# Kernel tuning notes

Measured on AMD Instinct MI355X. Metric: run time of the kernel, lower is better.

Reference implementation:

```python
import jax, jax.numpy as jnp
import numpy as np

N_NODES = 100000
N_EDGES = 1600000
N_CLUSTERS = 1024
EPS = 1e-5


def gcn_conv(x, W, b, src, dst, n, ew=None):
    """PyG GCNConv: symmetric norm with self-loops. ew: optional edge weight/mask."""
    h = x @ W
    if ew is None:
        ew = jnp.ones(src.shape[0], h.dtype)
    deg = jax.ops.segment_sum(ew, dst, num_segments=n) + 1.0  # +1 self loop
    dinv = jax.lax.rsqrt(deg)
    coef = dinv[src] * dinv[dst] * ew  # [E]
    out = jax.ops.segment_sum(h[src] * coef[:, None], dst, num_segments=n)
    out = out + h * (dinv * dinv)[:, None]  # self-loop messages
    return out + b


def instance_norm(x):
    # PyG InstanceNorm, batch=None -> single graph, no affine, biased variance
    mu = jnp.mean(x, axis=0, keepdims=True)
    var = jnp.mean((x - mu) ** 2, axis=0, keepdims=True)
    return (x - mu) * jax.lax.rsqrt(var + EPS)


def forward(x, WG1, bG1, WfG1, bfG1, WG2, bG2, WfG2, bfG2,
            WL1, bL1, WfL1, bfL1, WL2, bL2, WfL2, bfL2,
            WO1, bO1, WfO1, bfO1, WO2, bO2, WfO2, bfO2, WO3, bO3, WfO3, bfO3,
            adj, in_batch, cluster):
    elu = jax.nn.elu
    n = x.shape[0]
    src, dst = adj[0], adj[1]
    # global GCN stack
    h = elu(gcn_conv(x, WG1, bG1, src, dst, n))
    h = elu(h @ WfG1 + bfG1)
    h = elu(gcn_conv(h, WG2, bG2, src, dst, n))
    h = elu(h @ WfG2 + bfG2)
    y = instance_norm(h)  # [N, 256]
    # avg_pool over clusters (single graph -> batch offset is 0 but kept faithful)
    bc = cluster + in_batch * N_CLUSTERS  # [N]
    cnt = jax.ops.segment_sum(jnp.ones(n, y.dtype), bc, num_segments=N_CLUSTERS)
    px = jax.ops.segment_sum(y, bc, num_segments=N_CLUSTERS) / jnp.maximum(cnt, 1.0)[:, None]
    # pool edges: map through cluster, remove self-loops, coalesce (dedupe via sort+mask)
    psrc, pdst = bc[src], bc[dst]
    key = psrc * N_CLUSTERS + pdst
    order = jnp.argsort(key)
    ks = key[order]
    s2, d2 = psrc[order], pdst[order]
    first = jnp.concatenate([jnp.ones((1,), bool), ks[1:] != ks[:-1]])
    emask = (first & (s2 != d2)).astype(y.dtype)
    # local GCN stack on compressed graph
    lx = elu(gcn_conv(px, WL1, bL1, s2, d2, N_CLUSTERS, emask))
    lx = elu(lx @ WfL1 + bfL1)
    lx = elu(gcn_conv(lx, WL2, bL2, s2, d2, N_CLUSTERS, emask))
    lx = elu(lx @ WfL2 + bfL2)  # [C, 64]
    # gather-broadcast compressed features back to nodes
    comp = lx[bc]  # [N, 64]
    z = jnp.concatenate([y, comp], axis=1)  # [N, 320]
    z = elu(gcn_conv(z, WO1, bO1, src, dst, n))
    z = elu(z @ WfO1 + bfO1)
    z = elu(gcn_conv(z, WO2, bO2, src, dst, n))
    z = elu(z @ WfO2 + bfO2)
    z = elu(gcn_conv(z, WO3, bO3, src, dst, n))
    z = elu(z @ WfO3 + bfO3)
    return z


def _lin(key, i, o):
    k1, k2 = jax.random.split(key)
    s = 1.0 / np.sqrt(i)
    return (jax.random.normal(k1, (i, o), jnp.float32) * s,
            jax.random.normal(k2, (o,), jnp.float32) * s)


def setup_inputs() -> dict:
    key = jax.random.key(0)
    ks = jax.random.split(key, 20)
    inp = {}
    inp['x'] = jax.random.normal(ks[0], (N_NODES, 3), jnp.float32)
    inp['adj'] = jax.random.randint(ks[1], (2, N_EDGES), 0, N_NODES, jnp.int64 if jax.config.jax_enable_x64 else jnp.int32)
    inp['num_graphs'] = 1
    inp['in_batch'] = jnp.zeros((N_NODES,), jnp.int32)
    inp['cluster'] = jax.random.randint(ks[2], (N_NODES,), 0, N_CLUSTERS, jnp.int32)
    dims = [('G1', 3, 64), ('fG1', 64, 64), ('G2', 64, 256), ('fG2', 256, 256),
            ('L1', 256, 128), ('fL1', 128, 128), ('L2', 128, 64), ('fL2', 64, 64),
            ('O1', 320, 128), ('fO1', 128, 128), ('O2', 128, 32), ('fO2', 32, 32),
            ('O3', 32, 3), ('fO3', 3, 3)]
    for j, (name, i, o) in enumerate(dims):
        W, b = _lin(ks[3 + j], i, o)
        inp['W' + name] = W
        inp['b' + name] = b
    return inp


def reference(x, adj, num_graphs, in_batch, cluster,
              WG1, bG1, WfG1, bfG1, WG2, bG2, WfG2, bfG2,
              WL1, bL1, WfL1, bfL1, WL2, bL2, WfL2, bfL2,
              WO1, bO1, WfO1, bfO1, WO2, bO2, WfO2, bfO2, WO3, bO3, WfO3, bfO3):
    return forward(x, WG1, bG1, WfG1, bfG1, WG2, bG2, WfG2, bfG2,
                   WL1, bL1, WfL1, bfL1, WL2, bL2, WfL2, bfL2,
                   WO1, bO1, WfO1, bfO1, WO2, bO2, WfO2, bfO2,
                   WO3, bO3, WfO3, bfO3, adj, in_batch, cluster)
```

## Files before the change

kernel.cpp:

```cpp
#include <hip/hip_runtime.h>


#define NCLUST 1024

typedef short bf16x8 __attribute__((ext_vector_type(8)));
typedef float f32x4 __attribute__((ext_vector_type(4)));

__device__ __forceinline__ float elu1(float x) { return x > 0.f ? x : expm1f(x); }

__device__ __forceinline__ unsigned f2bf(float f) {
    union { float f; unsigned u; } c; c.f = f;
    unsigned u = c.u;
    return (u + 0x7fffu + ((u >> 16) & 1u)) >> 16;
}
__device__ __forceinline__ float bf2f(unsigned h) {
    union { unsigned u; float f; } c; c.u = h << 16; return c.f;
}

union U8 { unsigned u[4]; bf16x8 v; };

__device__ __forceinline__ void wpack_body(const float* W, unsigned* Phi, unsigned* Plo,
                                           int K, int BN, int t) {
    int NT = BN / 16;
    int lane = t & 63;
    int rest = t >> 6;
    int ct = rest % NT;
    int s = rest / NT;
    int col = ct * 16 + (lane & 15);
    int g = lane >> 4;
    int k0 = s * 32;
    float e[8];
#pragma unroll
    for (int j = 0; j < 4; j++) {
        e[j]     = W[(size_t)(k0 + 4 * g + j) * BN + col];
        e[4 + j] = W[(size_t)(k0 + 16 + 4 * g + j) * BN + col];
    }
#pragma unroll
    for (int j = 0; j < 4; j++) {
        unsigned h0 = f2bf(e[2 * j]), h1 = f2bf(e[2 * j + 1]);
        Phi[(size_t)t * 4 + j] = h0 | (h1 << 16);
        unsigned l0 = f2bf(e[2 * j] - bf2f(h0));
        unsigned l1 = f2bf(e[2 * j + 1] - bf2f(h1));
        Plo[(size_t)t * 4 + j] = l0 | (l1 << 16);
    }
}

struct PackDesc { const float* W; unsigned* Ph; unsigned* Pl; int K, BN, tbase; };
struct InitArgs {
    PackDesc d[6]; int tot;
    int4* z1; int nz1; int4* z2; int nz2;
};

__global__ void k_init(InitArgs a) {
    int t = blockIdx.x * 256 + threadIdx.x;
    if (t < a.nz1) a.z1[t] = make_int4(0, 0, 0, 0);
    else if (t - a.nz1 < a.nz2) a.z2[t - a.nz1] = make_int4(0, 0, 0, 0);
    if (t < a.tot) {
        int i = 0;
#pragma unroll
        for (int j = 1; j < 6; j++) if (t >= a.d[j].tbase) i = j;
        wpack_body(a.d[i].W, a.d[i].Ph, a.d[i].Pl, a.d[i].K, a.d[i].BN,
                   t - a.d[i].tbase);
    }
}

__global__ void k_hist(const int* __restrict__ key, int* __restrict__ deg, int E) {
    int e = blockIdx.x * 256 + threadIdx.x;
    if (e < E) atomicAdd(&deg[key[e]], 1);
}

__global__ void k_scan_block(const int* __restrict__ deg, int* __restrict__ rowptr,
                             int* __restrict__ bsum, int n) {
    __shared__ int lds[256];
    int tid = threadIdx.x;
    int base = blockIdx.x * 1024 + tid * 4;
    int v0 = base + 0 < n ? deg[base + 0] : 0;
    int v1 = base + 1 < n ? deg[base + 1] : 0;
    int v2 = base + 2 < n ? deg[base + 2] : 0;
    int v3 = base + 3 < n ? deg[base + 3] : 0;
    int tsum = v0 + v1 + v2 + v3;
    lds[tid] = tsum; __syncthreads();
    for (int off = 1; off < 256; off <<= 1) {
        int t = (tid >= off) ? lds[tid - off] : 0;
        __syncthreads();
        lds[tid] += t;
        __syncthreads();
    }
    int run = lds[tid] - tsum;
    if (base + 0 < n) rowptr[base + 0] = run; run += v0;
    if (base + 1 < n) rowptr[base + 1] = run; run += v1;
    if (base + 2 < n) rowptr[base + 2] = run; run += v2;
    if (base + 3 < n) rowptr[base + 3] = run;
    if (tid == 255) bsum[blockIdx.x] = lds[255];
}

__global__ void k_nodeinit(int* __restrict__ rowptr, const int* __restrict__ bsum,
                           const int* __restrict__ deg, const int* __restrict__ cluster,
                           const int* __restrict__ inb, float* __restrict__ dinv,
                           int* __restrict__ bc, int* __restrict__ cdeg, int n, int nb) {
    __shared__ int pfx[128];
    int tid = threadIdx.x;
    if (tid < 128) pfx[tid] = (tid < nb) ? bsum[tid] : 0;
    __syncthreads();
    for (int off = 1; off < 128; off <<= 1) {
        int v = 0;
        if (tid < 128 && tid >= off) v = pfx[tid - off];
        __syncthreads();
        if (tid < 128) pfx[tid] += v;
        __syncthreads();
    }
    int i = blockIdx.x * 256 + tid;
    if (i >= n) return;
    int j = i >> 10;
    int base = (j == 0) ? 0 : pfx[j - 1];
    rowptr[i] += base;
    dinv[i] = rsqrtf((float)deg[i] + 1.0f);
    int c = cluster[i] + inb[i] * NCLUST;
    bc[i] = c;
    atomicAdd(&cdeg[c], 1);
}

__global__ void k_fillc(const int* __restrict__ src, const int* __restrict__ dst,
                        const float* __restrict__ dinv, const int* __restrict__ rowptr,
                        int* __restrict__ fill, int2* __restrict__ csr_ev, int E,
                        const int* __restrict__ bc, const int* __restrict__ crowptr,
                        int* __restrict__ cfill, int* __restrict__ cnodes, int n) {
    int e = blockIdx.x * 256 + threadIdx.x;
    if (e < E) {
        int d = dst[e];
        int pos = rowptr[d] + atomicAdd(&fill[d], 1);
        int s = src[e];
        csr_ev[pos] = make_int2(s, __float_as_int(dinv[s]));
    }
    if (e < n) {
        int c = bc[e];
        int pos = crowptr[c] + atomicAdd(&cfill[c], 1);
        cnodes[pos] = e;
    }
}

template <int F, int OB>
__global__ __launch_bounds__(256) void k_prop4sb(
        const unsigned short* __restrict__ hbf, const float* __restrict__ dinv,
        const int* __restrict__ rowptr, const int* __restrict__ deg,
        const int2* __restrict__ csr_ev,
        const float* __restrict__ bias, float* __restrict__ outf,
        unsigned short* __restrict__ outb, int n, int flags) {
    constexpr int FS = F / 4;
    constexpr int ES = 64 / FS;
    const int node = (blockIdx.x * 256 + threadIdx.x) >> 6;
    if (node >= n) return;
    const int l = threadIdx.x & 63;
    const int fs = l & (FS - 1);
    const int ep = l / FS;
    const int fi = fs * 4;
    const int start = rowptr[node];
    const int cnt = deg[node];
    float ax = 0.f, ay = 0.f, az = 0.f, aw = 0.f;
    for (int j = ep; j < cnt; j += ES) {
        const int2 ev = csr_ev[start + j];
        int s = ev.x;
        float w = __int_as_float(ev.y);
        const ushort4 v = *reinterpret_cast<const ushort4*>(&hbf[(size_t)s * F + fi]);
        ax += w * bf2f(v.x); ay += w * bf2f(v.y);
        az += w * bf2f(v.z); aw += w * bf2f(v.w);
    }
#pragma unroll
    for (int off = FS; off < 64; off <<= 1) {
        ax += __shfl_xor(ax, off);
        ay += __shfl_xor(ay, off);
        az += __shfl_xor(az, off);
        aw += __shfl_xor(aw, off);
    }
    if (ep == 0) {
        float di = dinv[node];
        const ushort4 sv = *reinterpret_cast<const ushort4*>(&hbf[(size_t)node * F + fi]);
        float4 o;
        o.x = di * ax + di * di * bf2f(sv.x);
        o.y = di * ay + di * di * bf2f(sv.y);
        o.z = di * az + di * di * bf2f(sv.z);
        o.w = di * aw + di * di * bf2f(sv.w);
        if (flags) {
            const float4 b = *reinterpret_cast<const float4*>(&bias[fi]);
            o.x = elu1(o.x + b.x); o.y = elu1(o.y + b.y);
            o.z = elu1(o.z + b.z); o.w = elu1(o.w + b.w);
        }
        if constexpr (OB) {
            ushort4 ob;
            ob.x = (unsigned short)f2bf(o.x); ob.y = (unsigned short)f2bf(o.y);
            ob.z = (unsigned short)f2bf(o.z); ob.w = (unsigned short)f2bf(o.w);
            *reinterpret_cast<ushort4*>(&outb[(size_t)node * F + fi]) = ob;
        } else {
            *reinterpret_cast<float4*>(&outf[(size_t)node * F + fi]) = o;
        }
    }
}

__global__ void k_prop3f1(const float* __restrict__ h, const float* __restrict__ dinv,
                          const int* __restrict__ rowptr, const int* __restrict__ deg,
                          const int2* __restrict__ csr_ev,
                          const float* __restrict__ WG1, const float* __restrict__ bG1,
                          unsigned short* __restrict__ outb, int n) {
    int node = blockIdx.x * 256 + threadIdx.x;
    if (node >= n) return;
    int start = rowptr[node], cnt = deg[node];
    float a0 = 0.f, a1 = 0.f, a2 = 0.f;
    for (int j = 0; j < cnt; j++) {
        const int2 ev = csr_ev[start + j];
        int s = ev.x;
        float w = __int_as_float(ev.y);
        a0 += w * h[(size_t)s * 3 + 0];
        a1 += w * h[(size_t)s * 3 + 1];
        a2 += w * h[(size_t)s * 3 + 2];
    }
    float di = dinv[node];
    float p0 = di * a0 + di * di * h[(size_t)node * 3 + 0];
    float p1 = di * a1 + di * di * h[(size_t)node * 3 + 1];
    float p2 = di * a2 + di * di * h[(size_t)node * 3 + 2];
    unsigned short* op = outb + (size_t)node * 64;
#pragma unroll 4
    for (int c = 0; c < 64; c += 4) {
        ushort4 ob;
        ob.x = (unsigned short)f2bf(elu1(p0 * WG1[c + 0] + p1 * WG1[64 + c + 0] + p2 * WG1[128 + c + 0] + bG1[c + 0]));
        ob.y = (unsigned short)f2bf(elu1(p0 * WG1[c + 1] + p1 * WG1[64 + c + 1] + p2 * WG1[128 + c + 1] + bG1[c + 1]));
        ob.z = (unsigned short)f2bf(elu1(p0 * WG1[c + 2] + p1 * WG1[64 + c + 2] + p2 * WG1[128 + c + 2] + bG1[c + 2]));
        ob.w = (unsigned short)f2bf(elu1(p0 * WG1[c + 3] + p1 * WG1[64 + c + 3] + p2 * WG1[128 + c + 3] + bG1[c + 3]));
        *reinterpret_cast<ushort4*>(op + c) = ob;
    }
}

__global__ void k_prop3out(const float* __restrict__ h, const float* __restrict__ dinv,
                           const int* __restrict__ rowptr, const int* __restrict__ deg,
                           const int2* __restrict__ csr_ev,
                           const float* __restrict__ bO3, const float* __restrict__ WfO3,
                           const float* __restrict__ bfO3, float* __restrict__ out, int n) {
    int node = blockIdx.x * 256 + threadIdx.x;
    if (node >= n) return;
    int start = rowptr[node], cnt = deg[node];
    float a0 = 0.f, a1 = 0.f, a2 = 0.f;
    for (int j = 0; j < cnt; j++) {
        const int2 ev = csr_ev[start + j];
        int s = ev.x;
        float w = __int_as_float(ev.y);
        a0 += w * h[(size_t)s * 3 + 0];
        a1 += w * h[(size_t)s * 3 + 1];
        a2 += w * h[(size_t)s * 3 + 2];
    }
    float di = dinv[node];
    float o0 = elu1(di * a0 + di * di * h[(size_t)node * 3 + 0] + bO3[0]);
    float o1 = elu1(di * a1 + di * di * h[(size_t)node * 3 + 1] + bO3[1]);
    float o2 = elu1(di * a2 + di * di * h[(size_t)node * 3 + 2] + bO3[2]);
#pragma unroll
    for (int c = 0; c < 3; c++) {
        out[(size_t)node * 3 + c] =
            elu1(o0 * WfO3[c] + o1 * WfO3[3 + c] + o2 * WfO3[6 + c] + bfO3[c]);
    }
}

__global__ void k_normprep(const float* __restrict__ W, const float* __restrict__ insum,
                           const float* __restrict__ insumsq, unsigned* __restrict__ Phi,
                           unsigned* __restrict__ Plo, float* __restrict__ corr,
                           float* __restrict__ mu, float* __restrict__ rstd, int n) {
    const float fn = (float)n;
    const int bid = blockIdx.x, tid = threadIdx.x;
    if (bid == 16) {
        float m = insum[tid] / fn;
        float var = insumsq[tid] / fn - m * m;
        mu[tid] = m;
        rstd[tid] = rsqrtf(var + 1e-5f);
        return;
    }
    {
        int t = bid * 256 + tid;
        int lane = t & 63, rest = t >> 6;
        int ct = rest % 8, s = rest / 8;
        int col = ct * 16 + (lane & 15);
        int g = lane >> 4;
        int k0 = s * 32;
        float e[8];
#pragma unroll
        for (int j = 0; j < 4; j++) {
            int ka = k0 + 4 * g + j;
            int kb = k0 + 16 + 4 * g + j;
            float ma = insum[ka] / fn;
            float sa = rsqrtf(insumsq[ka] / fn - ma * ma + 1e-5f);
            float mb = insum[kb] / fn;
            float sb = rsqrtf(insumsq[kb] / fn - mb * mb + 1e-5f);
            e[j]     = W[(size_t)ka * 128 + col] * sa;
            e[4 + j] = W[(size_t)kb * 128 + col] * sb;
        }
#pragma unroll
        for (int j = 0; j < 4; j++) {
            unsigned h0 = f2bf(e[2 * j]), h1 = f2bf(e[2 * j + 1]);
            Phi[(size_t)t * 4 + j] = h0 | (h1 << 16);
            unsigned l0 = f2bf(e[2 * j] - bf2f(h0));
            unsigned l1 = f2bf(e[2 * j + 1] - bf2f(h1));
            Plo[(size_t)t * 4 + j] = l0 | (l1 << 16);
        }
    }
    if (tid < 128) {
        int k0 = bid * 16;
        float s = 0.f;
        for (int k = k0; k < k0 + 16; k++) {
            float m = insum[k] / fn;
            float r = rsqrtf(insumsq[k] / fn - m * m + 1e-5f);
            s += m * r * W[(size_t)k * 128 + tid];
        }
        atomicAdd(&corr[tid], s);
    }
}

template <int BN, int WAVES>
__global__ __launch_bounds__(WAVES * 64) void k_gmfma(
        const unsigned short* __restrict__ Abf,
        const unsigned* __restrict__ Phi, const unsigned* __restrict__ Plo,
        const float* __restrict__ bias, const float* __restrict__ sub,
        const float* __restrict__ add, const int* __restrict__ addidx,
        float* __restrict__ C, unsigned short* __restrict__ Cbf,
        int N, int K, int flags) {
    constexpr int NT = BN / 16;
    constexpr int WCOL = (BN == 256) ? 4 : (BN == 128 ? 2 : 1);
    constexpr int WROW = WAVES / WCOL;
    constexpr int NTW = NT / WCOL;
    constexpr int BR = 32 * WROW;
    constexpr bool LDSW = (BN >= 128);
    __shared__ unsigned lds_w[LDSW ? 2 * 2 * NT * 256 : 1];
    const int t = threadIdx.x;
    const int w = t >> 6, l = t & 63;
    const int wr = w / WCOL, wc = w % WCOL;
    const int l15 = l & 15, g = l >> 4;
    const int row0 = blockIdx.x * BR + wr * 32;
    const int ctbase = wc * NTW;
    int ar0 = row0 + l15;      ar0 = ar0 < N ? ar0 : N - 1;
    int ar1 = row0 + 16 + l15; ar1 = ar1 < N ? ar1 : N - 1;
    const unsigned short* ab0 = Abf + (size_t)ar0 * K;
    const unsigned short* ab1 = Abf + (size_t)ar1 * K;

    f32x4 acc[2][NTW];
#pragma unroll
    for (int f = 0; f < 2; f++)
#pragma unroll
        for (int ct = 0; ct < NTW; ct++) acc[f][ct] = (f32x4){0.f, 0.f, 0.f, 0.f};

    auto loadA = [&](int s, U8* ahi) {
        const int k0 = s * 32;
#pragma unroll
        for (int f = 0; f < 2; f++) {
            const unsigned short* ab = f ? ab1 : ab0;
            const uint2 hA = *reinterpret_cast<const uint2*>(ab + k0 + 4 * g);
            const uint2 hB = *reinterpret_cast<const uint2*>(ab + k0 + 16 + 4 * g);
            ahi[f].u[0] = hA.x; ahi[f].u[1] = hA.y;
            ahi[f].u[2] = hB.x; ahi[f].u[3] = hB.y;
        }
    };
    auto domfma = [&](U8* wh, U8* wl, U8* ahi) {
#pragma unroll
        for (int ct = 0; ct < NTW; ct++) {
            acc[0][ct] = __builtin_amdgcn_mfma_f32_16x16x32_bf16(ahi[0].v, wh[ct].v, acc[0][ct], 0, 0, 0);
            acc[0][ct] = __builtin_amdgcn_mfma_f32_16x16x32_bf16(ahi[0].v, wl[ct].v, acc[0][ct], 0, 0, 0);
            acc[1][ct] = __builtin_amdgcn_mfma_f32_16x16x32_bf16(ahi[1].v, wh[ct].v, acc[1][ct], 0, 0, 0);
            acc[1][ct] = __builtin_amdgcn_mfma_f32_16x16x32_bf16(ahi[1].v, wl[ct].v, acc[1][ct], 0, 0, 0);
        }
    };

    const int nk = K / 32;

    if constexpr (LDSW) {
        auto stage = [&](int s, int b) {
            unsigned* base = lds_w + (size_t)b * (2 * NT * 256);
            for (int i = w; i < 2 * NT; i += WAVES) {
                const unsigned* gsrc = (i < NT)
                    ? Phi + (size_t)(s * NT + i) * 256 + l * 4
                    : Plo + (size_t)(s * NT + (i - NT)) * 256 + l * 4;
                __builtin_amdgcn_global_load_lds(
                    (const __attribute__((address_space(1))) unsigned*)gsrc,
                    (__attribute__((address_space(3))) unsigned*)(base + i * 256),
                    16, 0, 0);
            }
        };
        auto loadWlds = [&](int b, U8* wh, U8* wl) {
            const unsigned* base = lds_w + (size_t)b * (2 * NT * 256);
#pragma unroll
            for (int ct = 0; ct < NTW; ct++) {
                wh[ct] = *reinterpret_cast<const U8*>(base + (ctbase + ct) * 256 + l * 4);
                wl[ct] = *reinterpret_cast<const U8*>(base + (NT + ctbase + ct) * 256 + l * 4);
            }
        };

        U8 wh[NTW], wl[NTW], ahiA[2], ahiB[2];
        stage(0, 0);
        loadA(0, ahiA);
        __syncthreads();
        int s = 0;
        while (true) {
            const bool hasB = (s + 1 < nk);
            if (hasB) { stage(s + 1, (s + 1) & 1); loadA(s + 1, ahiB); }
            loadWlds(s & 1, wh, wl);
            domfma(wh, wl, ahiA);
            __syncthreads();
            if (!hasB) break;
            s++;
            const bool hasA2 = (s + 1 < nk);
            if (hasA2) { stage(s + 1, (s + 1) & 1); loadA(s + 1, ahiA); }
            loadWlds(s & 1, wh, wl);
            domfma(wh, wl, ahiB);
            __syncthreads();
            if (!hasA2) break;
            s++;
        }
    } else {
        auto loadW = [&](int s, U8* wh, U8* wl) {
            const unsigned* pb = Phi + ((size_t)(s * NT + ctbase) * 64 + l) * 4;
            const unsigned* pl = Plo + ((size_t)(s * NT + ctbase) * 64 + l) * 4;
#pragma unroll
            for (int ct = 0; ct < NTW; ct++) {
                wh[ct] = *reinterpret_cast<const U8*>(pb + (size_t)ct * 256);
                wl[ct] = *reinterpret_cast<const U8*>(pl + (size_t)ct * 256);
            }
        };
        U8 whA[NTW], wlA[NTW], ahiA[2];
        U8 whB[NTW], wlB[NTW], ahiB[2];
        loadW(0, whA, wlA);
        loadA(0, ahiA);
        int s = 0;
        while (true) {
            const bool hasB = (s + 1 < nk);
            if (hasB) { loadW(s + 1, whB, wlB); loadA(s + 1, ahiB); }
            domfma(whA, wlA, ahiA);
            if (!hasB) break;
            const bool hasA2 = (s + 2 < nk);
            if (hasA2) { loadW(s + 2, whA, wlA); loadA(s + 2, ahiA); }
            domfma(whB, wlB, ahiB);
            if (!hasA2) break;
            s += 2;
        }
        __syncthreads();
    }

#pragma unroll
    for (int f = 0; f < 2; f++) {
#pragma unroll
        for (int r = 0; r < 4; r++) {
            int row = row0 + 16 * f + 4 * g + r;
            if (row >= N) continue;
            int gi = (add != nullptr) ? addidx[row] : 0;
#pragma unroll
            for (int ct = 0; ct < NTW; ct++) {
                int col = (ctbase + ct) * 16 + l15;
                float o = acc[f][ct][r];
                if (add != nullptr) o += add[(size_t)gi * BN + col];
                if (sub != nullptr) o -= sub[col];
                if (flags) o = elu1(o + bias[col]);
                if (C != nullptr) C[(size_t)row * BN + col] = o;
                if (Cbf != nullptr) Cbf[(size_t)row * BN + col] = (unsigned short)f2bf(o);
            }
        }
    }
}

template <int M, int RPT>
__global__ __launch_bounds__(256) void k_fc(
        const float* __restrict__ A, const float* __restrict__ W,
        const float* __restrict__ bias, const float* __restrict__ add,
        const int* __restrict__ addidx, float* __restrict__ C,
        int N, int K, int flags) {
    constexpr int TX = M / 4;
    constexpr int TY = 256 / TX;
    constexpr int RB = TY * RPT;
    int tx = threadIdx.x % TX;
    int ty = threadIdx.x / TX;
    int row0 = blockIdx.x * RB + ty * RPT;
    float4 acc[RPT];
#pragma unroll
    for (int r = 0; r < RPT; r++) acc[r] = make_float4(0.f, 0.f, 0.f, 0.f);
    for (int k = 0; k < K; k++) {
        float4 w = *reinterpret_cast<const float4*>(&W[(size_t)k * M + tx * 4]);
#pragma unroll
        for (int r = 0; r < RPT; r++) {
            int row = row0 + r;
            row = row < N ? row : N - 1;
            float a = A[(size_t)row * K + k];
            acc[r].x += a * w.x; acc[r].y += a * w.y;
            acc[r].z += a * w.z; acc[r].w += a * w.w;
        }
    }
    if (add != nullptr) {
#pragma unroll
        for (int r = 0; r < RPT; r++) {
            int row = row0 + r;
            if (row < N) {
                int g = addidx[row];
                const float4 v = *reinterpret_cast<const float4*>(&add[(size_t)g * M + tx * 4]);
                acc[r].x += v.x; acc[r].y += v.y; acc[r].z += v.z; acc[r].w += v.w;
            }
        }
    }
    __syncthreads();
    float4 b = make_float4(0.f, 0.f, 0.f, 0.f);
    if (flags) b = *reinterpret_cast<const float4*>(&bias[tx * 4]);
#pragma unroll
    for (int r = 0; r < RPT; r++) {
        int row = row0 + r;
        if (row >= N) break;
        float4 o = acc[r];
        o.x += b.x; o.y += b.y; o.z += b.z; o.w += b.w;
        if (flags) { o.x = elu1(o.x); o.y = elu1(o.y); o.z = elu1(o.z); o.w = elu1(o.w); }
        *reinterpret_cast<float4*>(&C[(size_t)row * M + tx * 4]) = o;
    }
}

__global__ __launch_bounds__(256) void k_fcl2(
        const float* __restrict__ A, const float* __restrict__ W1,
        const float* __restrict__ b1, const float* __restrict__ W2,
        float* __restrict__ lxout, float* __restrict__ compO) {
    __shared__ float lx[32][64];
    const int tid = threadIdx.x;
    const int tx = tid % 16, ty = tid / 16;
    const int row0b = blockIdx.x * 32;
    float4 acc[2];
    acc[0] = make_float4(0.f, 0.f, 0.f, 0.f);
    acc[1] = make_float4(0.f, 0.f, 0.f, 0.f);
    for (int k = 0; k < 64; k++) {
        float4 w = *reinterpret_cast<const float4*>(&W1[(size_t)k * 64 + tx * 4]);
#pragma unroll
        for (int r = 0; r < 2; r++) {
            float a = A[(size_t)(row0b + ty * 2 + r) * 64 + k];
            acc[r].x += a * w.x; acc[r].y += a * w.y;
            acc[r].z += a * w.z; acc[r].w += a * w.w;
        }
    }
    float4 b = *reinterpret_cast<const float4*>(&b1[tx * 4]);
#pragma unroll
    for (int r = 0; r < 2; r++) {
        int lr = ty * 2 + r;
        float4 o;
        o.x = elu1(acc[r].x + b.x); o.y = elu1(acc[r].y + b.y);
        o.z = elu1(acc[r].z + b.z); o.w = elu1(acc[r].w + b.w);
        *reinterpret_cast<float4*>(&lxout[(size_t)(row0b + lr) * 64 + tx * 4]) = o;
        lx[lr][tx * 4 + 0] = o.x; lx[lr][tx * 4 + 1] = o.y;
        lx[lr][tx * 4 + 2] = o.z; lx[lr][tx * 4 + 3] = o.w;
    }
    __syncthreads();
    for (int o = tid; o < 32 * 128; o += 256) {
        int r = o >> 7, c = o & 127;
        float s = 0.f;
        for (int k = 0; k < 64; k++) s += lx[r][k] * W2[(size_t)k * 128 + c];
        compO[(size_t)(row0b + r) * 128 + c] = s;
    }
}

__global__ void k_fc3(const float* __restrict__ A, const float* __restrict__ W,
                      const float* __restrict__ b, float* __restrict__ C,
                      int n, int K, int flags) {
    int r = blockIdx.x * 256 + threadIdx.x;
    if (r >= n) return;
    float a0 = 0.f, a1 = 0.f, a2 = 0.f;
    for (int k = 0; k < K; k++) {
        float a = A[(size_t)r * K + k];
        a0 += a * W[k * 3 + 0]; a1 += a * W[k * 3 + 1]; a2 += a * W[k * 3 + 2];
    }
    if (flags) {
        a0 = elu1(a0 + b[0]); a1 = elu1(a1 + b[1]); a2 = elu1(a2 + b[2]);
    }
    C[(size_t)r * 3 + 0] = a0;
    C[(size_t)r * 3 + 1] = a1;
    C[(size_t)r * 3 + 2] = a2;
}

__global__ void k_instats(const unsigned short* __restrict__ h, float* __restrict__ sum,
                          float* __restrict__ sumsq, int n) {
    int c = threadIdx.x;
    int r0 = blockIdx.x * 128;
    int r1 = r0 + 128 < n ? r0 + 128 : n;
    float s = 0.f, q = 0.f;
    for (int r = r0; r < r1; r++) {
        float v = bf2f(h[(size_t)r * 256 + c]);
        s += v; q += v * v;
    }
    atomicAdd(&sum[c], s);
    atomicAdd(&sumsq[c], q);
}

__global__ __launch_bounds__(256) void k_poolmerge(
        const unsigned short* __restrict__ xh, const int* __restrict__ crowptr,
        const int* __restrict__ cdeg, const int* __restrict__ cnodes,
        const float* __restrict__ mu, const float* __restrict__ rstd,
        float* __restrict__ px,
        const int* __restrict__ src, const int* __restrict__ dst,
        const int* __restrict__ bc, unsigned char* __restrict__ bmT, int E) {
    int bid = blockIdx.x;
    if (bid < NCLUST) {
        int cl = bid;
        int c  = threadIdx.x;
        int start = crowptr[cl];
        int cnt = cdeg[cl];
        float acc = 0.f;
        for (int j = 0; j < cnt; j++) {
            int node = cnodes[start + j];
            acc += bf2f(xh[(size_t)node * 256 + c]);
        }
        float res = acc / fmaxf((float)cnt, 1.0f);
        res = (cnt > 0) ? (res - mu[c]) * rstd[c] : 0.f;
        px[(size_t)cl * 256 + c] = res;
    } else {
        int e = (bid - NCLUST) * 256 + threadIdx.x;
        if (e < E) {
            int ps = bc[src[e]];
            int pd = bc[dst[e]];
            bmT[(size_t)pd * NCLUST + ps] = 1;
        }
    }
}

__global__ __launch_bounds__(256) void k_pooldeg(
        const unsigned char* __restrict__ bmT, float* __restrict__ dinvp) {
    int d = blockIdx.x;
    int t = threadIdx.x;
    const unsigned int v = reinterpret_cast<const unsigned int*>(bmT + (size_t)d * NCLUST)[t];
    int s = (v & 0xff) + ((v >> 8) & 0xff) + ((v >> 16) & 0xff) + ((v >> 24) & 0xff);
    if (t == (d >> 2)) s -= (v >> ((d & 3) * 8)) & 0xff;
    __shared__ int red[256];
    red[t] = s; __syncthreads();
    for (int o = 128; o > 0; o >>= 1) {
        if (t < o) red[t] += red[t + o];
        __syncthreads();
    }
    if (t == 0) dinvp[d] = rsqrtf((float)red[0] + 1.0f);
}

template <int F>
__global__ __launch_bounds__(1024) void k_proppool2(
        const float* __restrict__ h, const float* __restrict__ dinvp,
        const unsigned char* __restrict__ bmT, const float* __restrict__ bias,
        float* __restrict__ out) {
    constexpr int SG = 1024 / F;
    const int d = blockIdx.x;
    const int t = threadIdx.x;
    const int f = t & (F - 1);
    const int sg = t / F;
    const unsigned char* bmrow = bmT + (size_t)d * NCLUST;
    float acc = 0.f;
#pragma unroll 4
    for (int s = sg; s < NCLUST; s += SG) {
        float m = (s != d) ? (float)bmrow[s] : 0.f;
        acc += m * dinvp[s] * h[(size_t)s * F + f];
    }
    __shared__ float red[1024];
    red[t] = acc; __syncthreads();
#pragma unroll
    for (int o = SG / 2; o > 0; o >>= 1) {
        if (sg < o) red[t] += red[t + o * F];
        __syncthreads();
    }
    if (sg == 0) {
        float di = dinvp[d];
        float r = di * red[f] + di * di * h[(size_t)d * F + f] + bias[f];
        out[(size_t)d * F + f] = elu1(r);
    }
}

extern "C" void kernel_launch(void* const* d_in, const int* in_sizes, int n_in,
                              void* d_out, int out_size, void* d_ws, size_t ws_size,
                              hipStream_t stream) {
    const float* x       = (const float*)d_in[0];
    const int*   adj     = (const int*)d_in[1];
    const int*   inb     = (const int*)d_in[3];
    const int*   cluster = (const int*)d_in[4];
    const float* WG1  = (const float*)d_in[5];   const float* bG1  = (const float*)d_in[6];
    const float* WfG1 = (const float*)d_in[7];   const float* bfG1 = (const float*)d_in[8];
    const float* WG2  = (const float*)d_in[9];   const float* bG2  = (const float*)d_in[10];
    const float* WfG2 = (const float*)d_in[11];  const float* bfG2 = (const float*)d_in[12];
    const float* WL1  = (const float*)d_in[13];  const float* bL1  = (const float*)d_in[14];
    const float* WfL1 = (const float*)d_in[15];  const float* bfL1 = (const float*)d_in[16];
    const float* WL2  = (const float*)d_in[17];  const float* bL2  = (const float*)d_in[18];
    const float* WfL2 = (const float*)d_in[19];  const float* bfL2 = (const float*)d_in[20];
    const float* WO1  = (const float*)d_in[21];  const float* bO1  = (const float*)d_in[22];
    const float* WfO1 = (const float*)d_in[23];  const float* bfO1 = (const float*)d_in[24];
    const float* WO2  = (const float*)d_in[25];  const float* bO2  = (const float*)d_in[26];
    const float* WfO2 = (const float*)d_in[27];  const float* bfO2 = (const float*)d_in[28];
    const float* WO3  = (const float*)d_in[29];  const float* bO3  = (const float*)d_in[30];
    const float* WfO3 = (const float*)d_in[31];  const float* bfO3 = (const float*)d_in[32];
    float* out = (float*)d_out;

    const int n = in_sizes[0] / 3;
    const int E = in_sizes[1] / 2;
    const int* src = adj;
    const int* dst = adj + E;

    char* ws = (char*)d_ws;
    size_t off = 0;
    auto alloc = [&](size_t bytes) -> void* {
        void* p = ws + off;
        off = (off + bytes + 255) & ~(size_t)255;
        return p;
    };
    int*   deg     = (int*)alloc((size_t)n * 4);
    int*   fill    = (int*)alloc((size_t)n * 4);
    int*   cdeg    = (int*)alloc(NCLUST * 4);
    int*   cfill   = (int*)alloc(NCLUST * 4);
    int*   rowptr  = (int*)alloc((size_t)n * 4);
    int*   crowptr = (int*)alloc(NCLUST * 4);
    int*   cnodes  = (int*)alloc((size_t)n * 4);
    int*   bcarr   = (int*)alloc((size_t)n * 4);
    float* dinv    = (float*)alloc((size_t)n * 4);
    int*   bsum    = (int*)alloc(512);
    int2*  csr_ev  = (int2*)alloc((size_t)E * 8);
    float* X       = (float*)alloc((size_t)n * 256 * 4);
    unsigned short* Xh = (unsigned short*)alloc((size_t)n * 256 * 2);
    float* B       = (float*)alloc((size_t)n * 128 * 4);
    unsigned short* Bh = (unsigned short*)alloc((size_t)n * 128 * 2);
    float* insum   = (float*)alloc(256 * 4);
    float* insumsq = (float*)alloc(256 * 4);
    float* px      = (float*)alloc((size_t)NCLUST * 256 * 4);
    unsigned char* bmT = (unsigned char*)alloc((size_t)NCLUST * NCLUST);
    float* corr    = (float*)alloc(128 * 4);
    float* mu      = (float*)alloc(256 * 4);
    float* rstd    = (float*)alloc(256 * 4);
    float* dinvp   = (float*)alloc(NCLUST * 4);
    float* lA      = (float*)alloc((size_t)NCLUST * 128 * 4);
    float* lB      = (float*)alloc((size_t)NCLUST * 128 * 4);
    unsigned* pfG1h = (unsigned*)alloc(2048 * 4);   unsigned* pfG1l = (unsigned*)alloc(2048 * 4);
    unsigned* pG2h  = (unsigned*)alloc(8192 * 4);   unsigned* pG2l  = (unsigned*)alloc(8192 * 4);
    unsigned* pfG2h = (unsigned*)alloc(32768 * 4);  unsigned* pfG2l = (unsigned*)alloc(32768 * 4);
    unsigned* pO1h  = (unsigned*)alloc(16384 * 4);  unsigned* pO1l  = (unsigned*)alloc(16384 * 4);
    unsigned* pfO1h = (unsigned*)alloc(8192 * 4);   unsigned* pfO1l = (unsigned*)alloc(8192 * 4);
    unsigned* pO2h  = (unsigned*)alloc(2048 * 4);   unsigned* pO2l  = (unsigned*)alloc(2048 * 4);
    unsigned* pfO2h = (unsigned*)alloc(512 * 4);    unsigned* pfO2l = (unsigned*)alloc(512 * 4);
    (void)ws_size; (void)n_in; (void)out_size;

    unsigned short* Bh1 = Bh;
    unsigned short* Bh2 = Bh + (size_t)n * 64;

    auto cdiv = [](int a, int b) { return (a + b - 1) / b; };
    const int EB = cdiv(E, 256);
    const int PB = cdiv(n, 4);

    int nz1 = (int)(((char*)rowptr - (char*)deg) / 16);
    int nz2 = (int)(((char*)mu - (char*)insum) / 16);
    InitArgs ia;
    ia.d[0] = {WfG1, pfG1h, pfG1l, 64, 64, 0};
    ia.d[1] = {WG2,  pG2h,  pG2l,  64, 256, 512};
    ia.d[2] = {WfG2, pfG2h, pfG2l, 256, 256, 2560};
    ia.d[3] = {WfO1, pfO1h, pfO1l, 128, 128, 10752};
    ia.d[4] = {WO2,  pO2h,  pO2l,  128, 32, 12800};
    ia.d[5] = {WfO2, pfO2h, pfO2l, 32, 32, 13312};
    ia.tot = 13440;
    ia.z1 = (int4*)deg; ia.nz1 = nz1;
    ia.z2 = (int4*)insum; ia.nz2 = nz2;
    int initN = (nz1 + nz2 > ia.tot) ? (nz1 + nz2) : ia.tot;
    k_init<<<cdiv(initN, 256), 256, 0, stream>>>(ia);

    k_hist<<<EB, 256, 0, stream>>>(dst, deg, E);
    int nb = cdiv(n, 1024);
    k_scan_block<<<nb, 256, 0, stream>>>(deg, rowptr, bsum, n);
    k_nodeinit<<<cdiv(n, 256), 256, 0, stream>>>(rowptr, bsum, deg, cluster, inb,
                                                 dinv, bcarr, cdeg, n, nb);
    k_scan_block<<<1, 256, 0, stream>>>(cdeg, crowptr, bsum, NCLUST);
    k_fillc<<<EB, 256, 0, stream>>>(src, dst, dinv, rowptr, fill, csr_ev, E,
                                    bcarr, crowptr, cfill, cnodes, n);

    k_prop3f1<<<cdiv(n, 256), 256, 0, stream>>>(x, dinv, rowptr, deg, csr_ev,
                                                WG1, bG1, Bh1, n);
    k_gmfma<64, 8><<<cdiv(n, 256), 512, 0, stream>>>(Bh1, pfG1h, pfG1l, bfG1,
                                                     nullptr, nullptr, nullptr,
                                                     nullptr, Bh1, n, 64, 1);
    k_prop4sb<64, 1><<<PB, 256, 0, stream>>>(Bh1, dinv, rowptr, deg, csr_ev,
                                             nullptr, nullptr, Bh2, n, 0);
    k_gmfma<256, 8><<<cdiv(n, 64), 512, 0, stream>>>(Bh2, pG2h, pG2l, bG2,
                                                     nullptr, nullptr, nullptr,
                                                     nullptr, Xh, n, 64, 1);
    k_gmfma<256, 8><<<cdiv(n, 64), 512, 0, stream>>>(Xh, pfG2h, pfG2l, bfG2,
                                                     nullptr, nullptr, nullptr,
                                                     nullptr, Xh, n, 256, 1);

    k_instats<<<cdiv(n, 128), 256, 0, stream>>>(Xh, insum, insumsq, n);
    k_normprep<<<17, 256, 0, stream>>>(WO1, insum, insumsq, pO1h, pO1l, corr, mu, rstd, n);

    k_poolmerge<<<NCLUST + EB, 256, 0, stream>>>(Xh, crowptr, cdeg, cnodes, mu, rstd, px,
                                                 src, dst, bcarr, bmT, E);
    k_pooldeg<<<NCLUST, 256, 0, stream>>>(bmT, dinvp);

    k_fc<128, 2><<<cdiv(NCLUST, 16), 256, 0, stream>>>(px, WL1, nullptr, nullptr, nullptr,
                                                       lA, NCLUST, 256, 0);
    k_proppool2<128><<<NCLUST, 1024, 0, stream>>>(lA, dinvp, bmT, bL1, lB);
    k_fc<128, 2><<<cdiv(NCLUST, 16), 256, 0, stream>>>(lB, WfL1, bfL1, nullptr, nullptr,
                                                       lA, NCLUST, 128, 1);
    k_fc<64, 2><<<cdiv(NCLUST, 32), 256, 0, stream>>>(lA, WL2, nullptr, nullptr, nullptr,
                                                      lB, NCLUST, 128, 0);
    k_proppool2<64><<<NCLUST, 1024, 0, stream>>>(lB, dinvp, bmT, bL2, lA);
    k_fcl2<<<NCLUST / 32, 256, 0, stream>>>(lA, WfL2, bfL2, WO1 + (size_t)256 * 128,
                                            lB, lA);

    k_gmfma<128, 8><<<cdiv(n, 128), 512, 0, stream>>>(Xh, pO1h, pO1l, nullptr,
                                                      corr, lA, bcarr, nullptr, Bh,
                                                      n, 256, 0);
    k_prop4sb<128, 1><<<PB, 256, 0, stream>>>(Bh, dinv, rowptr, deg, csr_ev,
                                              bO1, nullptr, Xh, n, 1);
    k_gmfma<128, 8><<<cdiv(n, 128), 512, 0, stream>>>(Xh, pfO1h, pfO1l, bfO1,
                                                      nullptr, nullptr, nullptr,
                                                      nullptr, Xh, n, 128, 1);
    k_gmfma<32, 8><<<cdiv(n, 256), 512, 0, stream>>>(Xh, pO2h, pO2l, nullptr,
                                                     nullptr, nullptr, nullptr,
                                                     nullptr, Bh, n, 128, 0);
    k_prop4sb<32, 1><<<PB, 256, 0, stream>>>(Bh, dinv, rowptr, deg, csr_ev,
                                             bO2, nullptr, Xh, n, 1);
    k_gmfma<32, 8><<<cdiv(n, 256), 512, 0, stream>>>(Xh, pfO2h, pfO2l, bfO2,
                                                     nullptr, nullptr, nullptr,
                                                     X, nullptr, n, 32, 1);
    k_fc3<<<cdiv(n, 256), 256, 0, stream>>>(X, WO3, nullptr, B, n, 32, 0);
    k_prop3out<<<cdiv(n, 256), 256, 0, stream>>>(B, dinv, rowptr, deg, csr_ev,
                                                 bO3, WfO3, bfO3, out, n);
}
```

Measured before the change: 1.171 ms.

## Fuse final 32->3 linear into GEMM epilogue, enlarge GEMM blocks, unroll pooling loops

Folds the 32x3 projection into the epilogue of the preceding MFMA GEMM using a 16-lane shuffle reduction, removing the k_fc3 kernel and the fp32 intermediate write and reread. The 256- and 128-wide GEMMs now launch 16-wave blocks covering twice the rows, to reuse each staged weight tile across more rows. The instance-stats and cluster-pooling gathers are unrolled by four to expose more memory-level parallelism. Larger blocks may reduce occupancy or leave a partially filled tail.

Measured after the change: 1.147 ms. 1.02x faster.

```diff
diff --git a/kernel.cpp b/kernel.cpp
--- a/kernel.cpp
+++ b/kernel.cpp
@@ -317,6 +317,7 @@
         const float* __restrict__ bias, const float* __restrict__ sub,
         const float* __restrict__ add, const int* __restrict__ addidx,
         float* __restrict__ C, unsigned short* __restrict__ Cbf,
+        const float* __restrict__ W3, float* __restrict__ C3,
         int N, int K, int flags) {
     constexpr int NT = BN / 16;
     constexpr int WCOL = (BN == 256) ? 4 : (BN == 128 ? 2 : 1);
@@ -444,6 +445,7 @@
             int row = row0 + 16 * f + 4 * g + r;
             if (row >= N) continue;
             int gi = (add != nullptr) ? addidx[row] : 0;
+            float t0 = 0.f, t1 = 0.f, t2 = 0.f;
 #pragma unroll
             for (int ct = 0; ct < NTW; ct++) {
                 int col = (ctbase + ct) * 16 + l15;
@@ -453,6 +455,24 @@
                 if (flags) o = elu1(o + bias[col]);
                 if (C != nullptr) C[(size_t)row * BN + col] = o;
                 if (Cbf != nullptr) Cbf[(size_t)row * BN + col] = (unsigned short)f2bf(o);
+                if (W3 != nullptr) {
+                    t0 += o * W3[col * 3 + 0];
+                    t1 += o * W3[col * 3 + 1];
+                    t2 += o * W3[col * 3 + 2];
+                }
+            }
+            if (W3 != nullptr) {
+#pragma unroll
+                for (int m = 1; m < 16; m <<= 1) {
+                    t0 += __shfl_xor(t0, m);
+                    t1 += __shfl_xor(t1, m);
+                    t2 += __shfl_xor(t2, m);
+                }
+                if (l15 == 0) {
+                    C3[(size_t)row * 3 + 0] = t0;
+                    C3[(size_t)row * 3 + 1] = t1;
+                    C3[(size_t)row * 3 + 2] = t2;
+                }
             }
         }
     }
@@ -549,30 +569,13 @@
     }
 }
 
-__global__ void k_fc3(const float* __restrict__ A, const float* __restrict__ W,
-                      const float* __restrict__ b, float* __restrict__ C,
-                      int n, int K, int flags) {
-    int r = blockIdx.x * 256 + threadIdx.x;
-    if (r >= n) return;
-    float a0 = 0.f, a1 = 0.f, a2 = 0.f;
-    for (int k = 0; k < K; k++) {
-        float a = A[(size_t)r * K + k];
-        a0 += a * W[k * 3 + 0]; a1 += a * W[k * 3 + 1]; a2 += a * W[k * 3 + 2];
-    }
-    if (flags) {
-        a0 = elu1(a0 + b[0]); a1 = elu1(a1 + b[1]); a2 = elu1(a2 + b[2]);
-    }
-    C[(size_t)r * 3 + 0] = a0;
-    C[(size_t)r * 3 + 1] = a1;
-    C[(size_t)r * 3 + 2] = a2;
-}
-
 __global__ void k_instats(const unsigned short* __restrict__ h, float* __restrict__ sum,
                           float* __restrict__ sumsq, int n) {
     int c = threadIdx.x;
     int r0 = blockIdx.x * 128;
     int r1 = r0 + 128 < n ? r0 + 128 : n;
     float s = 0.f, q = 0.f;
+#pragma unroll 4
     for (int r = r0; r < r1; r++) {
         float v = bf2f(h[(size_t)r * 256 + c]);
         s += v; q += v * v;
@@ -595,7 +598,19 @@
         int start = crowptr[cl];
         int cnt = cdeg[cl];
         float acc = 0.f;
-        for (int j = 0; j < cnt; j++) {
+        int j = 0;
+        for (; j + 3 < cnt; j += 4) {
+            int n0 = cnodes[start + j + 0];
+            int n1 = cnodes[start + j + 1];
+            int n2 = cnodes[start + j + 2];
+            int n3 = cnodes[start + j + 3];
+            float v0 = bf2f(xh[(size_t)n0 * 256 + c]);
+            float v1 = bf2f(xh[(size_t)n1 * 256 + c]);
+            float v2 = bf2f(xh[(size_t)n2 * 256 + c]);
+            float v3 = bf2f(xh[(size_t)n3 * 256 + c]);
+            acc += (v0 + v1) + (v2 + v3);
+        }
+        for (; j < cnt; j++) {
             int node = cnodes[start + j];
             acc += bf2f(xh[(size_t)node * 256 + c]);
         }
@@ -763,15 +778,18 @@
                                                 WG1, bG1, Bh1, n);
     k_gmfma<64, 8><<<cdiv(n, 256), 512, 0, stream>>>(Bh1, pfG1h, pfG1l, bfG1,
                                                      nullptr, nullptr, nullptr,
-                                                     nullptr, Bh1, n, 64, 1);
+                                                     nullptr, Bh1, nullptr, nullptr,
+                                                     n, 64, 1);
     k_prop4sb<64, 1><<<PB, 256, 0, stream>>>(Bh1, dinv, rowptr, deg, csr_ev,
                                              nullptr, nullptr, Bh2, n, 0);
-    k_gmfma<256, 8><<<cdiv(n, 64), 512, 0, stream>>>(Bh2, pG2h, pG2l, bG2,
-                                                     nullptr, nullptr, nullptr,
-                                                     nullptr, Xh, n, 64, 1);
-    k_gmfma<256, 8><<<cdiv(n, 64), 512, 0, stream>>>(Xh, pfG2h, pfG2l, bfG2,
-                                                     nullptr, nullptr, nullptr,
-                                                     nullptr, Xh, n, 256, 1);
+    k_gmfma<256, 16><<<cdiv(n, 128), 1024, 0, stream>>>(Bh2, pG2h, pG2l, bG2,
+                                                        nullptr, nullptr, nullptr,
+                                                        nullptr, Xh, nullptr, nullptr,
+                                                        n, 64, 1);
+    k_gmfma<256, 16><<<cdiv(n, 128), 1024, 0, stream>>>(Xh, pfG2h, pfG2l, bfG2,
+                                                        nullptr, nullptr, nullptr,
+                                                        nullptr, Xh, nullptr, nullptr,
+                                                        n, 256, 1);
 
     k_instats<<<cdiv(n, 128), 256, 0, stream>>>(Xh, insum, insumsq, n);
     k_normprep<<<17, 256, 0, stream>>>(WO1, insum, insumsq, pO1h, pO1l, corr, mu, rstd, n);
@@ -791,23 +809,25 @@
     k_fcl2<<<NCLUST / 32, 256, 0, stream>>>(lA, WfL2, bfL2, WO1 + (size_t)256 * 128,
                                             lB, lA);
 
-    k_gmfma<128, 8><<<cdiv(n, 128), 512, 0, stream>>>(Xh, pO1h, pO1l, nullptr,
-                                                      corr, lA, bcarr, nullptr, Bh,
-                                                      n, 256, 0);
+    k_gmfma<128, 16><<<cdiv(n, 256), 1024, 0, stream>>>(Xh, pO1h, pO1l, nullptr,
+                                                        corr, lA, bcarr, nullptr, Bh,
+                                                        nullptr, nullptr, n, 256, 0);
     k_prop4sb<128, 1><<<PB, 256, 0, stream>>>(Bh, dinv, rowptr, deg, csr_ev,
                                               bO1, nullptr, Xh, n, 1);
-    k_gmfma<128, 8><<<cdiv(n, 128), 512, 0, stream>>>(Xh, pfO1h, pfO1l, bfO1,
-                                                      nullptr, nullptr, nullptr,
-                                                      nullptr, Xh, n, 128, 1);
+    k_gmfma<128, 16><<<cdiv(n, 256), 1024, 0, stream>>>(Xh, pfO1h, pfO1l, bfO1,
+                                                        nullptr, nullptr, nullptr,
+                                                        nullptr, Xh, nullptr, nullptr,
+                                                        n, 128, 1);
     k_gmfma<32, 8><<<cdiv(n, 256), 512, 0, stream>>>(Xh, pO2h, pO2l, nullptr,
                                                      nullptr, nullptr, nullptr,
-                                                     nullptr, Bh, n, 128, 0);
+                                                     nullptr, Bh, nullptr, nullptr,
+                                                     n, 128, 0);
     k_prop4sb<32, 1><<<PB, 256, 0, stream>>>(Bh, dinv, rowptr, deg, csr_ev,
                                              bO2, nullptr, Xh, n, 1);
     k_gmfma<32, 8><<<cdiv(n, 256), 512, 0, stream>>>(Xh, pfO2h, pfO2l, bfO2,
                                                      nullptr, nullptr, nullptr,
-                                                     X, nullptr, n, 32, 1);
-    k_fc3<<<cdiv(n, 256), 256, 0, stream>>>(X, WO3, nullptr, B, n, 32, 0);
+                                                     nullptr, nullptr, WO3, B,
+                                                     n, 32, 1);
     k_prop3out<<<cdiv(n, 256), 256, 0, stream>>>(B, dinv, rowptr, deg, csr_ev,
                                                  bO3, WfO3, bfO3, out, n);
 }
```
